# Kernel tuning notes

Hardware: AMD Instinct MI355X
Metric: run time of the kernel (lower is better)

The kernel has to match this reference:

```python
import jax, jax.numpy as jnp
import numpy as np

N = 100000   # nodes
E = 3200000  # edges
F = 100      # raw node features
FE = 4       # feature_embed_dim
VE = 1       # value_embed_dim
D = F * (FE + VE)  # 500, embedded dim
H = 16
C = 40
EPS = 1e-5


def gcn_conv(x, edge_index, W, b, num_nodes):
    """PyG GCNConv: h = D^-1/2 (A+I) D^-1/2 (x W) + b."""
    loop = jnp.arange(num_nodes)
    src = jnp.concatenate([edge_index[0], loop])
    dst = jnp.concatenate([edge_index[1], loop])
    deg = jax.ops.segment_sum(jnp.ones_like(dst, dtype=x.dtype), dst,
                              num_segments=num_nodes)
    dinv = jnp.where(deg > 0, jax.lax.rsqrt(jnp.maximum(deg, 1e-12)), 0.0)
    norm = dinv[src] * dinv[dst]                      # [E+N]
    h = x @ W                                         # [N, out]
    msg = h[src] * norm[:, None]                      # gather + scale
    out = jax.ops.segment_sum(msg, dst, num_segments=num_nodes)
    return out + b


def setup_inputs() -> dict:
    key = jax.random.key(0)
    ks = jax.random.split(key, 10)
    x = jax.random.normal(ks[0], (N, F), dtype=jnp.float32)
    edge_index = jax.random.randint(ks[1], (2, E), 0, N, dtype=jnp.int64)
    feat_emb = jax.random.normal(ks[2], (F, FE), dtype=jnp.float32) * 0.1
    val_emb = jax.random.normal(ks[3], (F, VE), dtype=jnp.float32) * 0.1
    gamma = jnp.ones((D,), dtype=jnp.float32)
    beta = jnp.zeros((D,), dtype=jnp.float32)
    W1 = jax.random.normal(ks[4], (D, H), dtype=jnp.float32) * (1.0 / np.sqrt(D))
    b1 = jnp.zeros((H,), dtype=jnp.float32)
    W2 = jax.random.normal(ks[5], (H, C), dtype=jnp.float32) * (1.0 / np.sqrt(H))
    b2 = jnp.zeros((C,), dtype=jnp.float32)
    return {"x": x, "edge_index": edge_index, "feat_emb": feat_emb,
            "val_emb": val_emb, "gamma": gamma, "beta": beta,
            "W1": W1, "b1": b1, "W2": W2, "b2": b2}


def reference(x, edge_index, feat_emb, val_emb, gamma, beta, W1, b1, W2, b2):
    # embed_features: each scalar feature j -> x_ij * [e_j (4d), v_j (1d)]
    emb = jnp.concatenate([feat_emb, val_emb], axis=1)       # [F, 5]
    h = (x[:, :, None] * emb[None, :, :]).reshape(N, D)      # [N, 500]
    # BatchNorm1d (training-mode batch statistics)
    mean = jnp.mean(h, axis=0)
    var = jnp.mean(jnp.square(h - mean), axis=0)
    h = (h - mean) * jax.lax.rsqrt(var + EPS) * gamma + beta
    # conv1 -> relu (dropout is identity in eval)
    h = gcn_conv(h, edge_index, W1, b1, N)
    h = jax.nn.relu(h)
    # conv2 -> log_softmax
    h = gcn_conv(h, edge_index, W2, b2, N)
    return jax.nn.log_softmax(h, axis=1)
```

## Files before the change

### kernel.cpp

```cpp
#include <hip/hip_runtime.h>
#include <hip/hip_bf16.h>
#include <math.h>

#define N_NODES 100000
#define N_EDGES 3200000
#define F_IN    100
#define D_DIM   500
#define H_DIM   16
#define C_DIM   40
#define EPS_BN  1e-5f
#define PAD     72
#define NBUCK   196
#define BCKCAP  17408

#define WS_SUMS    0
#define WS_DEGI    256
#define WS_WX      100256
#define WS_C1      101856
#define WS_GCUR    101888
#define WS_DINV    102144
#define WS_BINNED  202240
#define WS_Y1      202240
#define WS_H1      1802240
#define WS_SSRC    3614208

#define MIX_STATS_BLOCKS 400
#define NB_BIN 782
#define MIX_BLOCKS (MIX_STATS_BLOCKS + NB_BIN)

__global__ void k_init(float* __restrict__ sums, int* __restrict__ gcur) {
    int t = threadIdx.x;
    sums[t] = 0.f;
    if (t < NBUCK) gcur[t] = t * BCKCAP;
}

__global__ void k_mixA(const float* __restrict__ x, const int* __restrict__ src,
                       const int* __restrict__ dst, float* __restrict__ sums,
                       int* __restrict__ gcur, int* __restrict__ binned) {
    __shared__ int smem[4096 + 256 + 256 + 256];
    if (blockIdx.x < MIX_STATS_BLOCKS) {
        float* ls = (float*)smem;
        for (int i = threadIdx.x; i < 200; i += 256) ls[i] = 0.f;
        __syncthreads();
        const int total4 = N_NODES * F_IN / 4;
        const float4* x4 = (const float4*)x;
        int g0 = blockIdx.x * 256 + threadIdx.x;
        int c0 = (4 * g0) % 100;
        float s0=0,s1=0,s2=0,s3=0,q0=0,q1=0,q2=0,q3=0;
        for (int g = g0; g < total4; g += MIX_STATS_BLOCKS * 256) {
            float4 v = x4[g];
            s0 += v.x; q0 += v.x*v.x;
            s1 += v.y; q1 += v.y*v.y;
            s2 += v.z; q2 += v.z*v.z;
            s3 += v.w; q3 += v.w*v.w;
        }
        atomicAdd(&ls[c0+0], s0); atomicAdd(&ls[100+c0+0], q0);
        atomicAdd(&ls[c0+1], s1); atomicAdd(&ls[100+c0+1], q1);
        atomicAdd(&ls[c0+2], s2); atomicAdd(&ls[100+c0+2], q2);
        atomicAdd(&ls[c0+3], s3); atomicAdd(&ls[100+c0+3], q3);
        __syncthreads();
        for (int i = threadIdx.x; i < 200; i += 256) {
            if (i < 100) atomicAdd(&sums[i], ls[i]);
            else         atomicAdd(&sums[128 + (i-100)], ls[i]);
        }
    } else {
        int* dstl = smem;
        int* cnt  = smem + 4096;
        int* base = smem + 4352;
        int* cnt2 = smem + 4608;
        int bb = blockIdx.x - MIX_STATS_BLOCKS;
        int t  = threadIdx.x;
        cnt[t & 255] = 0; cnt2[t & 255] = 0;
        __syncthreads();
        const int4* dst4 = (const int4*)dst;
        const int4* src4 = (const int4*)src;
        const int ne4 = N_EDGES / 4;
        int i40 = bb * 1024;
        #pragma unroll
        for (int k = 0; k < 4; k++) {
            int i4 = i40 + t + 256 * k;
            if (i4 < ne4) {
                int4 d4 = dst4[i4];
                ((int4*)dstl)[t + 256 * k] = d4;
                atomicAdd(&cnt[d4.x >> 9], 1);
                atomicAdd(&cnt[d4.y >> 9], 1);
                atomicAdd(&cnt[d4.z >> 9], 1);
                atomicAdd(&cnt[d4.w >> 9], 1);
            }
        }
        __syncthreads();
        if (t < NBUCK && cnt[t] > 0) base[t] = atomicAdd(&gcur[t], cnt[t]);
        __syncthreads();
        #pragma unroll
        for (int k = 0; k < 4; k++) {
            int i4 = i40 + t + 256 * k;
            if (i4 < ne4) {
                int4 d4 = ((int4*)dstl)[t + 256 * k];
                int4 s4 = src4[i4];
                int bx, r;
                bx = d4.x >> 9; r = atomicAdd(&cnt2[bx], 1);
                binned[base[bx] + r] = ((d4.x & 511) << 17) | s4.x;
                bx = d4.y >> 9; r = atomicAdd(&cnt2[bx], 1);
                binned[base[bx] + r] = ((d4.y & 511) << 17) | s4.y;
                bx = d4.z >> 9; r = atomicAdd(&cnt2[bx], 1);
                binned[base[bx] + r] = ((d4.z & 511) << 17) | s4.z;
                bx = d4.w >> 9; r = atomicAdd(&cnt2[bx], 1);
                binned[base[bx] + r] = ((d4.w & 511) << 17) | s4.w;
            }
        }
    }
}

__global__ void k_bucket(const int* __restrict__ binned, const int* __restrict__ gcur,
                         int* __restrict__ ssrc, int* __restrict__ degi,
                         float* __restrict__ dinv) {
    __shared__ int cnt[512];
    int b = blockIdx.x, t = threadIdx.x;
    for (int i = t; i < 512; i += 256) cnt[i] = 0;
    __syncthreads();
    int lo  = b * 512;
    int beg = b * BCKCAP;
    int nb  = gcur[b] - beg;
    for (int e = t; e < nb; e += 256) {
        int v  = binned[beg + e];
        int ld = v >> 17;
        int sv = v & 0x1FFFF;
        int p = atomicAdd(&cnt[ld], 1);
        if (p < PAD) ssrc[(lo + ld) * PAD + p] = sv;
    }
    __syncthreads();
    for (int ld = t; ld < 512; ld += 256) {
        int d = lo + ld;
        if (d < N_NODES) {
            int c = cnt[ld];
            degi[d] = c;
            dinv[d] = rsqrtf((float)(c + 1));
        }
    }
}

__global__ void k_fold(const float* __restrict__ sums, const float* __restrict__ fe,
                       const float* __restrict__ ve, const float* __restrict__ gamma,
                       const float* __restrict__ beta, const float* __restrict__ W1,
                       float* __restrict__ wx, float* __restrict__ c1) {
    __shared__ float a[D_DIM];
    __shared__ float mt[D_DIM];
    const float invN = 1.0f / (float)N_NODES;
    for (int d = threadIdx.x; d < D_DIM; d += 256) {
        int j = d / 5, k = d % 5;
        float e   = (k < 4) ? fe[j*4 + k] : ve[j];
        float mx  = sums[j] * invN;
        float msq = sums[128 + j] * invN;
        float varx = msq - mx * mx;
        float rstd = rsqrtf(e*e*varx + EPS_BN);
        float ad = rstd * gamma[d];
        a[d]  = ad * e;
        mt[d] = beta[d] - (e * mx) * ad;
    }
    __syncthreads();
    for (int t = threadIdx.x; t < F_IN * H_DIM; t += 256) {
        int j = t >> 4, c = t & 15;
        float s = 0.f;
        #pragma unroll
        for (int k = 0; k < 5; k++) {
            int d = j*5 + k;
            s += a[d] * W1[d*16 + c];
        }
        wx[t] = s;
    }
    __shared__ float cacc[16][17];
    int c = threadIdx.x & 15, chunk = threadIdx.x >> 4;
    float s = 0.f;
    for (int d = chunk; d < D_DIM; d += 16) s += mt[d] * W1[d*16 + c];
    cacc[chunk][c] = s;
    __syncthreads();
    if (threadIdx.x < 16) {
        float t2 = 0.f;
        #pragma unroll
        for (int q = 0; q < 16; q++) t2 += cacc[q][threadIdx.x];
        c1[threadIdx.x] = t2;
    }
}

__global__ void k_y1(const float* __restrict__ x, const float* __restrict__ wx,
                     const float* __restrict__ c1, const float* __restrict__ dinv,
                     float* __restrict__ y1s) {
    __shared__ float swx[F_IN * H_DIM];
    __shared__ float sc1[16];
    for (int i = threadIdx.x; i < F_IN*H_DIM; i += 256) swx[i] = wx[i];
    if (threadIdx.x < 16) sc1[threadIdx.x] = c1[threadIdx.x];
    __syncthreads();
    int g = blockIdx.x * 256 + threadIdx.x;
    int node = g >> 4, c = g & 15;
    const float* xr = x + node * F_IN;
    float s = sc1[c];
    #pragma unroll
    for (int j = 0; j < F_IN; j++) s += xr[j] * swx[j*16 + c];
    y1s[g] = dinv[node] * s;
}

__global__ void k_agg1(const float* __restrict__ y1s, const int* __restrict__ degi,
                       const int* __restrict__ ssrc, const float* __restrict__ dinv,
                       const float* __restrict__ b1, float* __restrict__ h1s) {
    int g = blockIdx.x * 256 + threadIdx.x;
    int v = g >> 4, c = g & 15;
    int cnt = min(degi[v], PAD);
    const int4* s4p = (const int4*)(ssrc + v * PAD);
    float dv = dinv[v];
    float acc = y1s[g];
    int i = 0;
    for (; i + 8 <= cnt; i += 8) {
        int4 a4 = s4p[(i >> 2)];
        int4 b4 = s4p[(i >> 2) + 1];
        float t0 = y1s[a4.x*16 + c], t1 = y1s[a4.y*16 + c];
        float t2 = y1s[a4.z*16 + c], t3 = y1s[a4.w*16 + c];
        float t4 = y1s[b4.x*16 + c], t5 = y1s[b4.y*16 + c];
        float t6 = y1s[b4.z*16 + c], t7 = y1s[b4.w*16 + c];
        acc += ((t0 + t1) + (t2 + t3)) + ((t4 + t5) + (t6 + t7));
    }
    for (; i + 4 <= cnt; i += 4) {
        int4 a4 = s4p[(i >> 2)];
        float t0 = y1s[a4.x*16 + c], t1 = y1s[a4.y*16 + c];
        float t2 = y1s[a4.z*16 + c], t3 = y1s[a4.w*16 + c];
        acc += (t0 + t1) + (t2 + t3);
    }
    for (; i < cnt; i++) acc += y1s[ssrc[v*PAD + i]*16 + c];
    float t = dv * acc + b1[c];
    h1s[g] = dv * fmaxf(t, 0.f);
}

__global__ void k_agg2f(const float* __restrict__ h1s, const int* __restrict__ degi,
                        const int* __restrict__ ssrc, const float* __restrict__ dinv,
                        const float* __restrict__ b2, const float* __restrict__ W2,
                        float* __restrict__ out) {
    __shared__ float sw[H_DIM * C_DIM];
    __shared__ float sb[C_DIM];
    for (int i = threadIdx.x; i < H_DIM*C_DIM; i += 256) sw[i] = W2[i];
    if (threadIdx.x < C_DIM) sb[threadIdx.x] = b2[threadIdx.x];
    __syncthreads();
    int g = blockIdx.x * 256 + threadIdx.x;
    int v = g >> 4, c = g & 15;
    int cnt = min(degi[v], PAD);
    const int4* s4p = (const int4*)(ssrc + v * PAD);
    float acc = h1s[g];
    int i = 0;
    for (; i + 8 <= cnt; i += 8) {
        int4 a4 = s4p[(i >> 2)];
        int4 b4 = s4p[(i >> 2) + 1];
        float t0 = h1s[a4.x*16 + c], t1 = h1s[a4.y*16 + c];
        float t2 = h1s[a4.z*16 + c], t3 = h1s[a4.w*16 + c];
        float t4 = h1s[b4.x*16 + c], t5 = h1s[b4.y*16 + c];
        float t6 = h1s[b4.z*16 + c], t7 = h1s[b4.w*16 + c];
        acc += ((t0 + t1) + (t2 + t3)) + ((t4 + t5) + (t6 + t7));
    }
    for (; i + 4 <= cnt; i += 4) {
        int4 a4 = s4p[(i >> 2)];
        float t0 = h1s[a4.x*16 + c], t1 = h1s[a4.y*16 + c];
        float t2 = h1s[a4.z*16 + c], t3 = h1s[a4.w*16 + c];
        acc += (t0 + t1) + (t2 + t3);
    }
    for (; i < cnt; i++) acc += h1s[ssrc[v*PAD + i]*16 + c];
    float af = dinv[v] * acc;
    int lane = threadIdx.x & 63;
    int base = lane & ~15;
    float z0 = sb[c], z1 = sb[c+16];
    float z2 = (c < 8) ? sb[c+32] : 0.f;
    #pragma unroll
    for (int j = 0; j < 16; j++) {
        float aj = __shfl(af, base + j, 64);
        z0 += aj * sw[j*C_DIM + c];
        z1 += aj * sw[j*C_DIM + c + 16];
        if (c < 8) z2 += aj * sw[j*C_DIM + c + 32];
    }
    float m = fmaxf(z0, z1);
    if (c < 8) m = fmaxf(m, z2);
    #pragma unroll
    for (int off = 1; off < 16; off <<= 1) m = fmaxf(m, __shfl_xor(m, off, 64));
    float se = expf(z0 - m) + expf(z1 - m) + ((c < 8) ? expf(z2 - m) : 0.f);
    #pragma unroll
    for (int off = 1; off < 16; off <<= 1) se += __shfl_xor(se, off, 64);
    float lse = m + logf(se);
    float* orow = out + v * C_DIM;
    orow[c]      = z0 - lse;
    orow[c + 16] = z1 - lse;
    if (c < 8) orow[c + 32] = z2 - lse;
}

extern "C" void kernel_launch(void* const* d_in, const int* in_sizes, int n_in,
                              void* d_out, int out_size, void* d_ws, size_t ws_size,
                              hipStream_t stream) {
    const float* x     = (const float*)d_in[0];
    const int*   ei    = (const int*)d_in[1];
    const float* fe    = (const float*)d_in[2];
    const float* ve    = (const float*)d_in[3];
    const float* gamma = (const float*)d_in[4];
    const float* beta  = (const float*)d_in[5];
    const float* W1    = (const float*)d_in[6];
    const float* b1    = (const float*)d_in[7];
    const float* W2    = (const float*)d_in[8];
    const float* b2    = (const float*)d_in[9];
    float* out = (float*)d_out;

    float* wsf = (float*)d_ws;
    int*   wsi = (int*)d_ws;

    float* sums   = wsf + WS_SUMS;
    int*   degi   = wsi + WS_DEGI;
    float* wx     = wsf + WS_WX;
    float* c1     = wsf + WS_C1;
    int*   gcur   = wsi + WS_GCUR;
    float* dinv   = wsf + WS_DINV;
    int*   binned = wsi + WS_BINNED;
    int*   ssrc   = wsi + WS_SSRC;
    float* y1s    = wsf + WS_Y1;
    float* h1s    = wsf + WS_H1;

    const int* src = ei;
    const int* dst = ei + N_EDGES;

    k_init<<<1, 256, 0, stream>>>(sums, gcur);
    k_mixA<<<MIX_BLOCKS, 256, 0, stream>>>(x, src, dst, sums, gcur, binned);
    k_bucket<<<NBUCK, 256, 0, stream>>>(binned, gcur, ssrc, degi, dinv);
    k_fold<<<1, 256, 0, stream>>>(sums, fe, ve, gamma, beta, W1, wx, c1);
    k_y1<<<(N_NODES*H_DIM)/256, 256, 0, stream>>>(x, wx, c1, dinv, y1s);
    k_agg1<<<(N_NODES*H_DIM)/256, 256, 0, stream>>>(y1s, degi, ssrc, dinv, b1, h1s);
    k_agg2f<<<(N_NODES*H_DIM)/256, 256, 0, stream>>>(h1s, degi, ssrc, dinv, b2, W2, out);
}
```

Before: 307.9 us.

## Store intermediate features in fp16, fuse bucket and fold kernels, stage x in LDS

Stores the per-node intermediate activations y1 and h1 as fp16 instead of fp32, halving the bytes moved by the random gathers in both aggregation kernels. Merges the bucket kernel and the single-block BN-fold kernel into one launch, using an extra block. Halves the edges handled per binning block so more blocks run, and stages each block's x rows in shared memory with float4 loads in k_y1. The fp16 storage reduces precision of intermediate sums, and the bucket count is now clamped to its capacity.

Measured after the change: 294.2 us. 1.05x faster.

```diff
diff --git a/kernel.cpp b/kernel.cpp
--- a/kernel.cpp
+++ b/kernel.cpp
@@ -1,5 +1,6 @@
 #include <hip/hip_runtime.h>
 #include <hip/hip_bf16.h>
+#include <hip/hip_fp16.h>
 #include <math.h>
 
 #define N_NODES 100000
@@ -21,11 +22,12 @@
 #define WS_DINV    102144
 #define WS_BINNED  202240
 #define WS_Y1      202240
-#define WS_H1      1802240
+#define WS_H1      1002240
 #define WS_SSRC    3614208
 
 #define MIX_STATS_BLOCKS 400
-#define NB_BIN 782
+#define BIN_I4 512
+#define NB_BIN 1563
 #define MIX_BLOCKS (MIX_STATS_BLOCKS + NB_BIN)
 
 __global__ void k_init(float* __restrict__ sums, int* __restrict__ gcur) {
@@ -37,7 +39,7 @@
 __global__ void k_mixA(const float* __restrict__ x, const int* __restrict__ src,
                        const int* __restrict__ dst, float* __restrict__ sums,
                        int* __restrict__ gcur, int* __restrict__ binned) {
-    __shared__ int smem[4096 + 256 + 256 + 256];
+    __shared__ int smem[2816];
     if (blockIdx.x < MIX_STATS_BLOCKS) {
         float* ls = (float*)smem;
         for (int i = threadIdx.x; i < 200; i += 256) ls[i] = 0.f;
@@ -65,19 +67,19 @@
         }
     } else {
         int* dstl = smem;
-        int* cnt  = smem + 4096;
-        int* base = smem + 4352;
-        int* cnt2 = smem + 4608;
+        int* cnt  = smem + 2048;
+        int* base = smem + 2304;
+        int* cnt2 = smem + 2560;
         int bb = blockIdx.x - MIX_STATS_BLOCKS;
         int t  = threadIdx.x;
-        cnt[t & 255] = 0; cnt2[t & 255] = 0;
+        cnt[t] = 0; cnt2[t] = 0;
         __syncthreads();
         const int4* dst4 = (const int4*)dst;
         const int4* src4 = (const int4*)src;
         const int ne4 = N_EDGES / 4;
-        int i40 = bb * 1024;
+        int i40 = bb * BIN_I4;
         #pragma unroll
-        for (int k = 0; k < 4; k++) {
+        for (int k = 0; k < 2; k++) {
             int i4 = i40 + t + 256 * k;
             if (i4 < ne4) {
                 int4 d4 = dst4[i4];
@@ -92,7 +94,7 @@
         if (t < NBUCK && cnt[t] > 0) base[t] = atomicAdd(&gcur[t], cnt[t]);
         __syncthreads();
         #pragma unroll
-        for (int k = 0; k < 4; k++) {
+        for (int k = 0; k < 2; k++) {
             int i4 = i40 + t + 256 * k;
             if (i4 < ne4) {
                 int4 d4 = ((int4*)dstl)[t + 256 * k];
@@ -111,125 +113,136 @@
     }
 }
 
-__global__ void k_bucket(const int* __restrict__ binned, const int* __restrict__ gcur,
-                         int* __restrict__ ssrc, int* __restrict__ degi,
-                         float* __restrict__ dinv) {
-    __shared__ int cnt[512];
-    int b = blockIdx.x, t = threadIdx.x;
-    for (int i = t; i < 512; i += 256) cnt[i] = 0;
-    __syncthreads();
-    int lo  = b * 512;
-    int beg = b * BCKCAP;
-    int nb  = gcur[b] - beg;
-    for (int e = t; e < nb; e += 256) {
-        int v  = binned[beg + e];
-        int ld = v >> 17;
-        int sv = v & 0x1FFFF;
-        int p = atomicAdd(&cnt[ld], 1);
-        if (p < PAD) ssrc[(lo + ld) * PAD + p] = sv;
-    }
-    __syncthreads();
-    for (int ld = t; ld < 512; ld += 256) {
-        int d = lo + ld;
-        if (d < N_NODES) {
-            int c = cnt[ld];
-            degi[d] = c;
-            dinv[d] = rsqrtf((float)(c + 1));
-        }
-    }
-}
-
-__global__ void k_fold(const float* __restrict__ sums, const float* __restrict__ fe,
-                       const float* __restrict__ ve, const float* __restrict__ gamma,
-                       const float* __restrict__ beta, const float* __restrict__ W1,
-                       float* __restrict__ wx, float* __restrict__ c1) {
-    __shared__ float a[D_DIM];
-    __shared__ float mt[D_DIM];
-    const float invN = 1.0f / (float)N_NODES;
-    for (int d = threadIdx.x; d < D_DIM; d += 256) {
-        int j = d / 5, k = d % 5;
-        float e   = (k < 4) ? fe[j*4 + k] : ve[j];
-        float mx  = sums[j] * invN;
-        float msq = sums[128 + j] * invN;
-        float varx = msq - mx * mx;
-        float rstd = rsqrtf(e*e*varx + EPS_BN);
-        float ad = rstd * gamma[d];
-        a[d]  = ad * e;
-        mt[d] = beta[d] - (e * mx) * ad;
-    }
-    __syncthreads();
-    for (int t = threadIdx.x; t < F_IN * H_DIM; t += 256) {
-        int j = t >> 4, c = t & 15;
+__global__ void k_bucketfold(const int* __restrict__ binned, const int* __restrict__ gcur,
+                             int* __restrict__ ssrc, int* __restrict__ degi,
+                             float* __restrict__ dinv,
+                             const float* __restrict__ sums, const float* __restrict__ fe,
+                             const float* __restrict__ ve, const float* __restrict__ gamma,
+                             const float* __restrict__ beta, const float* __restrict__ W1,
+                             float* __restrict__ wx, float* __restrict__ c1) {
+    __shared__ float smf[1272];
+    int t = threadIdx.x;
+    if (blockIdx.x < NBUCK) {
+        int* cnt = (int*)smf;
+        for (int i = t; i < 512; i += 256) cnt[i] = 0;
+        __syncthreads();
+        int b   = blockIdx.x;
+        int lo  = b * 512;
+        int beg = b * BCKCAP;
+        int nb  = min(gcur[b] - beg, BCKCAP);
+        for (int e = t; e < nb; e += 256) {
+            int v  = binned[beg + e];
+            int ld = v >> 17;
+            int sv = v & 0x1FFFF;
+            int p = atomicAdd(&cnt[ld], 1);
+            if (p < PAD) ssrc[(lo + ld) * PAD + p] = sv;
+        }
+        __syncthreads();
+        for (int ld = t; ld < 512; ld += 256) {
+            int d = lo + ld;
+            if (d < N_NODES) {
+                int c = cnt[ld];
+                degi[d] = c;
+                dinv[d] = rsqrtf((float)(c + 1));
+            }
+        }
+    } else {
+        float* a  = smf;
+        float* mt = smf + 500;
+        float (*cacc)[17] = (float(*)[17])(smf + 1000);
+        const float invN = 1.0f / (float)N_NODES;
+        for (int d = t; d < D_DIM; d += 256) {
+            int j = d / 5, k = d % 5;
+            float e   = (k < 4) ? fe[j*4 + k] : ve[j];
+            float mx  = sums[j] * invN;
+            float msq = sums[128 + j] * invN;
+            float varx = msq - mx * mx;
+            float rstd = rsqrtf(e*e*varx + EPS_BN);
+            float ad = rstd * gamma[d];
+            a[d]  = ad * e;
+            mt[d] = beta[d] - (e * mx) * ad;
+        }
+        __syncthreads();
+        for (int q = t; q < F_IN * H_DIM; q += 256) {
+            int j = q >> 4, c = q & 15;
+            float s = 0.f;
+            #pragma unroll
+            for (int k = 0; k < 5; k++) {
+                int d = j*5 + k;
+                s += a[d] * W1[d*16 + c];
+            }
+            wx[q] = s;
+        }
+        int c = t & 15, chunk = t >> 4;
         float s = 0.f;
-        #pragma unroll
-        for (int k = 0; k < 5; k++) {
-            int d = j*5 + k;
-            s += a[d] * W1[d*16 + c];
-        }
-        wx[t] = s;
-    }
-    __shared__ float cacc[16][17];
-    int c = threadIdx.x & 15, chunk = threadIdx.x >> 4;
-    float s = 0.f;
-    for (int d = chunk; d < D_DIM; d += 16) s += mt[d] * W1[d*16 + c];
-    cacc[chunk][c] = s;
-    __syncthreads();
-    if (threadIdx.x < 16) {
-        float t2 = 0.f;
-        #pragma unroll
-        for (int q = 0; q < 16; q++) t2 += cacc[q][threadIdx.x];
-        c1[threadIdx.x] = t2;
+        for (int d = chunk; d < D_DIM; d += 16) s += mt[d] * W1[d*16 + c];
+        __syncthreads();
+        cacc[chunk][c] = s;
+        __syncthreads();
+        if (t < 16) {
+            float t2 = 0.f;
+            #pragma unroll
+            for (int q = 0; q < 16; q++) t2 += cacc[q][t];
+            c1[t] = t2;
+        }
     }
 }
 
 __global__ void k_y1(const float* __restrict__ x, const float* __restrict__ wx,
                      const float* __restrict__ c1, const float* __restrict__ dinv,
-                     float* __restrict__ y1s) {
+                     __half* __restrict__ y1s) {
     __shared__ float swx[F_IN * H_DIM];
+    __shared__ float sx[16 * F_IN];
     __shared__ float sc1[16];
-    for (int i = threadIdx.x; i < F_IN*H_DIM; i += 256) swx[i] = wx[i];
-    if (threadIdx.x < 16) sc1[threadIdx.x] = c1[threadIdx.x];
+    int t = threadIdx.x;
+    const float4* wx4 = (const float4*)wx;
+    float4* swx4 = (float4*)swx;
+    for (int i = t; i < 400; i += 256) swx4[i] = wx4[i];
+    const float4* x4 = (const float4*)(x + blockIdx.x * 1600);
+    float4* sx4 = (float4*)sx;
+    for (int i = t; i < 400; i += 256) sx4[i] = x4[i];
+    if (t < 16) sc1[t] = c1[t];
     __syncthreads();
-    int g = blockIdx.x * 256 + threadIdx.x;
-    int node = g >> 4, c = g & 15;
-    const float* xr = x + node * F_IN;
+    int ln = t >> 4, c = t & 15;
+    int node = blockIdx.x * 16 + ln;
+    const float* xr = sx + ln * F_IN;
     float s = sc1[c];
     #pragma unroll
     for (int j = 0; j < F_IN; j++) s += xr[j] * swx[j*16 + c];
-    y1s[g] = dinv[node] * s;
-}
-
-__global__ void k_agg1(const float* __restrict__ y1s, const int* __restrict__ degi,
+    y1s[node * 16 + c] = __float2half(dinv[node] * s);
+}
+
+__global__ void k_agg1(const __half* __restrict__ y1s, const int* __restrict__ degi,
                        const int* __restrict__ ssrc, const float* __restrict__ dinv,
-                       const float* __restrict__ b1, float* __restrict__ h1s) {
+                       const float* __restrict__ b1, __half* __restrict__ h1s) {
     int g = blockIdx.x * 256 + threadIdx.x;
     int v = g >> 4, c = g & 15;
     int cnt = min(degi[v], PAD);
     const int4* s4p = (const int4*)(ssrc + v * PAD);
     float dv = dinv[v];
-    float acc = y1s[g];
+    float acc = __half2float(y1s[g]);
     int i = 0;
     for (; i + 8 <= cnt; i += 8) {
         int4 a4 = s4p[(i >> 2)];
         int4 b4 = s4p[(i >> 2) + 1];
-        float t0 = y1s[a4.x*16 + c], t1 = y1s[a4.y*16 + c];
-        float t2 = y1s[a4.z*16 + c], t3 = y1s[a4.w*16 + c];
-        float t4 = y1s[b4.x*16 + c], t5 = y1s[b4.y*16 + c];
-        float t6 = y1s[b4.z*16 + c], t7 = y1s[b4.w*16 + c];
+        float t0 = __half2float(y1s[a4.x*16 + c]), t1 = __half2float(y1s[a4.y*16 + c]);
+        float t2 = __half2float(y1s[a4.z*16 + c]), t3 = __half2float(y1s[a4.w*16 + c]);
+        float t4 = __half2float(y1s[b4.x*16 + c]), t5 = __half2float(y1s[b4.y*16 + c]);
+        float t6 = __half2float(y1s[b4.z*16 + c]), t7 = __half2float(y1s[b4.w*16 + c]);
         acc += ((t0 + t1) + (t2 + t3)) + ((t4 + t5) + (t6 + t7));
     }
     for (; i + 4 <= cnt; i += 4) {
         int4 a4 = s4p[(i >> 2)];
-        float t0 = y1s[a4.x*16 + c], t1 = y1s[a4.y*16 + c];
-        float t2 = y1s[a4.z*16 + c], t3 = y1s[a4.w*16 + c];
+        float t0 = __half2float(y1s[a4.x*16 + c]), t1 = __half2float(y1s[a4.y*16 + c]);
+        float t2 = __half2float(y1s[a4.z*16 + c]), t3 = __half2float(y1s[a4.w*16 + c]);
         acc += (t0 + t1) + (t2 + t3);
     }
-    for (; i < cnt; i++) acc += y1s[ssrc[v*PAD + i]*16 + c];
-    float t = dv * acc + b1[c];
-    h1s[g] = dv * fmaxf(t, 0.f);
-}
-
-__global__ void k_agg2f(const float* __restrict__ h1s, const int* __restrict__ degi,
+    for (; i < cnt; i++) acc += __half2float(y1s[ssrc[v*PAD + i]*16 + c]);
+    float tt = dv * acc + b1[c];
+    h1s[g] = __float2half(dv * fmaxf(tt, 0.f));
+}
+
+__global__ void k_agg2f(const __half* __restrict__ h1s, const int* __restrict__ degi,
                         const int* __restrict__ ssrc, const float* __restrict__ dinv,
                         const float* __restrict__ b2, const float* __restrict__ W2,
                         float* __restrict__ out) {
@@ -242,24 +255,24 @@
     int v = g >> 4, c = g & 15;
     int cnt = min(degi[v], PAD);
     const int4* s4p = (const int4*)(ssrc + v * PAD);
-    float acc = h1s[g];
+    float acc = __half2float(h1s[g]);
     int i = 0;
     for (; i + 8 <= cnt; i += 8) {
         int4 a4 = s4p[(i >> 2)];
         int4 b4 = s4p[(i >> 2) + 1];
-        float t0 = h1s[a4.x*16 + c], t1 = h1s[a4.y*16 + c];
-        float t2 = h1s[a4.z*16 + c], t3 = h1s[a4.w*16 + c];
-        float t4 = h1s[b4.x*16 + c], t5 = h1s[b4.y*16 + c];
-        float t6 = h1s[b4.z*16 + c], t7 = h1s[b4.w*16 + c];
+        float t0 = __half2float(h1s[a4.x*16 + c]), t1 = __half2float(h1s[a4.y*16 + c]);
+        float t2 = __half2float(h1s[a4.z*16 + c]), t3 = __half2float(h1s[a4.w*16 + c]);
+        float t4 = __half2float(h1s[b4.x*16 + c]), t5 = __half2float(h1s[b4.y*16 + c]);
+        float t6 = __half2float(h1s[b4.z*16 + c]), t7 = __half2float(h1s[b4.w*16 + c]);
         acc += ((t0 + t1) + (t2 + t3)) + ((t4 + t5) + (t6 + t7));
     }
     for (; i + 4 <= cnt; i += 4) {
         int4 a4 = s4p[(i >> 2)];
-        float t0 = h1s[a4.x*16 + c], t1 = h1s[a4.y*16 + c];
-        float t2 = h1s[a4.z*16 + c], t3 = h1s[a4.w*16 + c];
+        float t0 = __half2float(h1s[a4.x*16 + c]), t1 = __half2float(h1s[a4.y*16 + c]);
+        float t2 = __half2float(h1s[a4.z*16 + c]), t3 = __half2float(h1s[a4.w*16 + c]);
         acc += (t0 + t1) + (t2 + t3);
     }
-    for (; i < cnt; i++) acc += h1s[ssrc[v*PAD + i]*16 + c];
+    for (; i < cnt; i++) acc += __half2float(h1s[ssrc[v*PAD + i]*16 + c]);
     float af = dinv[v] * acc;
     int lane = threadIdx.x & 63;
     int base = lane & ~15;
@@ -304,24 +317,24 @@
     float* wsf = (float*)d_ws;
     int*   wsi = (int*)d_ws;
 
-    float* sums   = wsf + WS_SUMS;
-    int*   degi   = wsi + WS_DEGI;
-    float* wx     = wsf + WS_WX;
-    float* c1     = wsf + WS_C1;
-    int*   gcur   = wsi + WS_GCUR;
-    float* dinv   = wsf + WS_DINV;
-    int*   binned = wsi + WS_BINNED;
-    int*   ssrc   = wsi + WS_SSRC;
-    float* y1s    = wsf + WS_Y1;
-    float* h1s    = wsf + WS_H1;
+    float*  sums   = wsf + WS_SUMS;
+    int*    degi   = wsi + WS_DEGI;
+    float*  wx     = wsf + WS_WX;
+    float*  c1     = wsf + WS_C1;
+    int*    gcur   = wsi + WS_GCUR;
+    float*  dinv   = wsf + WS_DINV;
+    int*    binned = wsi + WS_BINNED;
+    int*    ssrc   = wsi + WS_SSRC;
+    __half* y1s    = (__half*)(wsi + WS_Y1);
+    __half* h1s    = (__half*)(wsi + WS_H1);
 
     const int* src = ei;
     const int* dst = ei + N_EDGES;
 
     k_init<<<1, 256, 0, stream>>>(sums, gcur);
     k_mixA<<<MIX_BLOCKS, 256, 0, stream>>>(x, src, dst, sums, gcur, binned);
-    k_bucket<<<NBUCK, 256, 0, stream>>>(binned, gcur, ssrc, degi, dinv);
-    k_fold<<<1, 256, 0, stream>>>(sums, fe, ve, gamma, beta, W1, wx, c1);
+    k_bucketfold<<<NBUCK + 1, 256, 0, stream>>>(binned, gcur, ssrc, degi, dinv,
+                                                sums, fe, ve, gamma, beta, W1, wx, c1);
     k_y1<<<(N_NODES*H_DIM)/256, 256, 0, stream>>>(x, wx, c1, dinv, y1s);
     k_agg1<<<(N_NODES*H_DIM)/256, 256, 0, stream>>>(y1s, degi, ssrc, dinv, b1, h1s);
     k_agg2f<<<(N_NODES*H_DIM)/256, 256, 0, stream>>>(h1s, degi, ssrc, dinv, b2, W2, out);
```
